# Kernel tuning notes

Hardware: AMD Instinct MI355X
Metric: run time of the kernel (lower is better)

Reference implementation:

```python
import jax, jax.numpy as jnp
import numpy as np
from jax import lax

B, C, H, W = 16, 128, 128, 128
K = 3
EPS = 1e-8


def setup_inputs() -> dict:
    key = jax.random.key(0)
    k1, k2, k3 = jax.random.split(key, 3)
    x = jax.random.normal(k1, (B, C, H, W), dtype=jnp.float32)
    style = jax.random.normal(k2, (B, C), dtype=jnp.float32)
    weight = jax.random.normal(k3, (C, C, K, K), dtype=jnp.float32)
    return {"x": x, "style": style, "weight": weight}


def reference(x, style, weight):
    b = x.shape[0]
    o, i, kh, kw = weight.shape
    h, w_sp = x.shape[2], x.shape[3]
    # style / ||style||_inf over channel dim (per-sample scalar)
    s = style / jnp.max(jnp.abs(style), axis=1, keepdims=True)          # (B, i)
    # weight * (1/sqrt(i*kh*kw)) / ||weight||_inf over (i,kh,kw) per out channel
    wmax = jnp.max(jnp.abs(weight), axis=(1, 2, 3), keepdims=True)      # (o,1,1,1)
    wn = weight * (1.0 / jnp.sqrt(jnp.float32(i * kh * kw)) / wmax)     # (o,i,kh,kw)
    # per-sample modulation over input channels
    wmod = wn[None] * s[:, None, :, None, None]                         # (B,o,i,kh,kw)
    # demodulation (coe reshaped to (i,1,1,1) in torch; valid since o==i)
    coe = lax.rsqrt(jnp.sum(jnp.square(wmod), axis=(2, 3, 4)) + EPS)    # (B,o)
    wmod = wmod * coe[:, :, None, None, None]
    # fused batched conv via grouped-conv trick (StyleGAN2-style)
    xr = x.reshape(1, b * i, h, w_sp)
    wr = wmod.reshape(b * o, i, kh, kw)
    out = lax.conv_general_dilated(
        xr, wr,
        window_strides=(1, 1),
        padding=[(1, 1), (1, 1)],
        feature_group_count=b,
        dimension_numbers=("NCHW", "OIHW", "NCHW"),
    )
    return out.reshape(b, o, h, w_sp)
```

## Files before the change

kernel.cpp:

```cpp
#include <hip/hip_runtime.h>
#include <hip/hip_bf16.h>


#define BATCH 16
#define CH    128
#define HW    128
#define WPITCH 1152

#define WS_WMAX 0
#define WS_SN   128
#define WS_AFAC 2176
#define WS_WT   4224
#define WFRAG_BYTE_OFF 606720
#define WFRAG_BYTES    4718592
#define WS_NEEDED      (WFRAG_BYTE_OFF + WFRAG_BYTES)

typedef short  s8v  __attribute__((ext_vector_type(8)));
typedef float  f4v  __attribute__((ext_vector_type(4)));
typedef float  f2v  __attribute__((ext_vector_type(2)));

__device__ inline unsigned short f2bf(float f) {
    union { float f; unsigned int u; } v; v.f = f;
    unsigned int r = v.u + 0x7FFFu + ((v.u >> 16) & 1u);
    return (unsigned short)(r >> 16);
}

__global__ __launch_bounds__(256) void kprep(const float* __restrict__ style,
                                             const float* __restrict__ weight,
                                             unsigned short* __restrict__ wfrag) {
    const int b  = blockIdx.x >> 3;
    const int mo = blockIdx.x & 7;
    const int t  = threadIdx.x;

    __shared__ float wrow[16 * 1153];
    __shared__ float snl[128];
    __shared__ float afl[16];
    __shared__ float red[4];

    float sv = (t < 128) ? style[b * CH + t] : 0.f;
    float m = fabsf(sv);
    #pragma unroll
    for (int off = 32; off > 0; off >>= 1)
        m = fmaxf(m, __shfl_down(m, off, 64));
    if ((t & 63) == 0) red[t >> 6] = m;

    for (int idx = t; idx < 16 * 1152; idx += 256) {
        int r = idx / 1152;
        int c = idx - r * 1152;
        wrow[r * 1153 + c] = weight[(size_t)(mo * 16 + r) * WPITCH + c];
    }
    __syncthreads();
    float smax = fmaxf(fmaxf(red[0], red[1]), fmaxf(red[2], red[3]));
    if (t < 128) snl[t] = sv / smax;
    __syncthreads();

    const int o16 = t >> 4;
    const int s   = t & 15;
    float mx = 0.f, ss = 0.f;
    for (int c = s; c < 1152; c += 16) {
        float v = wrow[o16 * 1153 + c];
        mx = fmaxf(mx, fabsf(v));
        float u = v * snl[c / 9];
        ss += u * u;
    }
    #pragma unroll
    for (int off = 8; off > 0; off >>= 1) {
        mx = fmaxf(mx, __shfl_down(mx, off, 16));
        ss += __shfl_down(ss, off, 16);
    }
    if (s == 0) {
        float scale = 1.0f / (sqrtf(1152.0f) * mx);
        afl[o16] = scale * rsqrtf(scale * scale * ss + 1e-8f);
    }
    __syncthreads();

    for (int fid = t; fid < 2304; fid += 256) {
        const int lane = fid & 63;
        int f2 = fid >> 6;
        const int ci = f2 & 3;
        const int kk = f2 >> 2;
        const int ro = lane & 15;
        const int i0 = ci * 32 + (lane >> 4) * 8;
        const float af = afl[ro];
        union { unsigned short u[8]; uint4 v; } pk;
        #pragma unroll
        for (int j = 0; j < 8; ++j) {
            int i = i0 + j;
            float v = wrow[ro * 1153 + i * 9 + kk] * af * snl[i];
            pk.u[j] = f2bf(v);
        }
        *(uint4*)(wfrag + ((size_t)(((b * 9 + kk) * 4 + ci) * 8 + mo) * 64 + lane) * 8) = pk.v;
    }
}

#define XBUF 16640

__device__ inline int xoff(int r, int c, int qs) { return (r * 130 + c) * 32 + qs * 8; }

__device__ inline const s8v* afrag_ptr(const unsigned short* wfrag, int b, int kk,
                                       int ci, int mo, int lane) {
    return (const s8v*)(wfrag + ((size_t)(((b * 9 + kk) * 4 + ci) * 8 + mo) * 64 + lane) * 8);
}

__global__ __launch_bounds__(512, 1) void k4_mfma(const float* __restrict__ x,
                                                  const unsigned short* __restrict__ wfrag,
                                                  float* __restrict__ out) {
    const int wg  = blockIdx.x;
    const int swz = (wg & 7) * 128 + (wg >> 3);
    const int b   = swz >> 6;
    const int h0  = (swz & 63) * 2;

    const int t    = threadIdx.x;
    const int lane = t & 63;
    const int wid  = t >> 6;
    const int oq    = wid & 3;
    const int rsel  = wid >> 2;
    const int ln15  = lane & 15;
    const int quad  = lane >> 4;

    __shared__ unsigned short xls[2 * XBUF];

    if (t < 64) {
        const int zb = (t >> 5) & 1;
        const int zr = (t >> 3) & 3;
        const int zc = ((t >> 2) & 1) ? 129 : 0;
        const int zq = t & 3;
        *(s8v*)&xls[zb * XBUF + xoff(zr, zc, zq)] = (s8v){0, 0, 0, 0, 0, 0, 0, 0};
    }

    f4v acc[2][8];
    #pragma unroll
    for (int mt = 0; mt < 2; ++mt)
        #pragma unroll
        for (int nt = 0; nt < 8; ++nt)
            acc[mt][nt] = (f4v){0.f, 0.f, 0.f, 0.f};

    const int  cp     = lane;
    const int  sr     = wid & 3;
    const int  hs     = wid >> 2;
    const int  it0    = hs * 2;
    const int  it1    = hs * 2 + 1;
    const int  srow   = h0 - 1 + sr;
    const bool svalid = (unsigned)srow < 128u;
    const int  srcl   = svalid ? srow : 0;

    #pragma unroll
    for (int k = 0; k < 2; ++k) {
        const int it = it0 + k;
        const float* xp = x + (((size_t)(b * CH + it * 8)) * HW + srcl) * HW + 2 * cp;
        union { unsigned short u[16]; s8v v[2]; } pk;
        #pragma unroll
        for (int j = 0; j < 8; ++j) {
            f2v d = *(const f2v*)(xp + (size_t)j * HW * HW);
            pk.u[j]     = f2bf(svalid ? d.x : 0.f);
            pk.u[8 + j] = f2bf(svalid ? d.y : 0.f);
        }
        *(s8v*)&xls[xoff(sr, 2 * cp + 1, it ^ (cp & 3))]       = pk.v[0];
        *(s8v*)&xls[xoff(sr, 2 * cp + 2, it ^ ((cp + 1) & 3))] = pk.v[1];
    }
    __syncthreads();

#define ISSUE(IT) do { \
    const float* xp_ = x + (((size_t)(b * CH + ibn + (IT) * 8)) * HW + srcl) * HW + 2 * cp; \
    _Pragma("unroll") \
    for (int j = 0; j < 8; ++j) pf[j] = *(const f2v*)(xp_ + (size_t)j * HW * HW); \
} while (0)

#define COMMIT(IT) do { \
    union { unsigned short u[16]; s8v v[2]; } pk_; \
    _Pragma("unroll") \
    for (int j = 0; j < 8; ++j) { \
        pk_.u[j]     = f2bf(svalid ? pf[j].x : 0.f); \
        pk_.u[8 + j] = f2bf(svalid ? pf[j].y : 0.f); } \
    *(s8v*)&bufn[xoff(sr, 2 * cp + 1, (IT) ^ (cp & 3))]       = pk_.v[0]; \
    *(s8v*)&bufn[xoff(sr, 2 * cp + 2, (IT) ^ ((cp + 1) & 3))] = pk_.v[1]; \
} while (0)

    s8v aN[2];
    #pragma unroll
    for (int mt = 0; mt < 2; ++mt)
        aN[mt] = *afrag_ptr(wfrag, b, 0, 0, oq * 2 + mt, lane);

    #pragma unroll 1
    for (int ci = 0; ci < 4; ++ci) {
        unsigned short* bufc = xls + (ci & 1) * XBUF;
        unsigned short* bufn = xls + ((ci & 1) ^ 1) * XBUF;
        const int ibn = (ci + 1) * 32;
        f2v pf[8];

        #pragma unroll
        for (int kk = 0; kk < 9; ++kk) {
            s8v aC[2];
            #pragma unroll
            for (int mt = 0; mt < 2; ++mt) aC[mt] = aN[mt];
            {
                const int pci = (kk < 8) ? ci : ci + 1;
                const int pkk = (kk < 8) ? kk + 1 : 0;
                if (pci < 4) {
                    #pragma unroll
                    for (int mt = 0; mt < 2; ++mt)
                        aN[mt] = *afrag_ptr(wfrag, b, pkk, pci, oq * 2 + mt, lane);
                }
            }
            if (ci < 3) {
                if      (kk == 0) { ISSUE(it0); }
                else if (kk == 4) { COMMIT(it0); ISSUE(it1); }
                else if (kk == 8) { COMMIT(it1); }
            }
            const int ky = kk / 3;
            const int kx = kk - ky * 3;
            const int r  = rsel + ky;
            s8v bf[8];
            #pragma unroll
            for (int nt = 0; nt < 8; ++nt) {
                const int c = nt * 16 + ln15 + kx;
                bf[nt] = *(const s8v*)&bufc[xoff(r, c, quad ^ ((c >> 1) & 3))];
            }
            #pragma unroll
            for (int mt = 0; mt < 2; ++mt)
                #pragma unroll
                for (int nt = 0; nt < 8; ++nt)
                    acc[mt][nt] = __builtin_amdgcn_mfma_f32_16x16x32_bf16(
                        aC[mt], bf[nt], acc[mt][nt], 0, 0, 0);
        }
        __syncthreads();
    }
#undef ISSUE
#undef COMMIT

    const int orow = h0 + rsel;
    #pragma unroll
    for (int mt = 0; mt < 2; ++mt) {
        int o = oq * 32 + mt * 16 + quad * 4;
        #pragma unroll
        for (int nt = 0; nt < 8; ++nt) {
            int xcol = nt * 16 + ln15;
            float* op = out + (((size_t)(b * CH + o)) * HW + orow) * HW + xcol;
            #pragma unroll
            for (int reg = 0; reg < 4; ++reg)
                op[(size_t)reg * HW * HW] = acc[mt][nt][reg];
        }
    }
}

__global__ __launch_bounds__(256) void k0_transpose(const float* __restrict__ w,
                                                    float* __restrict__ ws) {
    int idx = blockIdx.x * 256 + threadIdx.x;
    if (idx < CH * WPITCH) {
        int kt = idx >> 7;
        int o  = idx & 127;
        ws[WS_WT + idx] = w[(size_t)o * WPITCH + kt];
    }
}

__global__ __launch_bounds__(256) void k1_norms(const float* __restrict__ style,
                                                const float* __restrict__ weight,
                                                float* __restrict__ ws) {
    __shared__ float red[4];
    const int bid = blockIdx.x;
    const int t = threadIdx.x;
    if (bid < 128) {
        const int o = bid;
        float m = 0.f;
        for (int idx = t; idx < WPITCH; idx += 256)
            m = fmaxf(m, fabsf(weight[(size_t)o * WPITCH + idx]));
        #pragma unroll
        for (int off = 32; off > 0; off >>= 1)
            m = fmaxf(m, __shfl_down(m, off, 64));
        if ((t & 63) == 0) red[t >> 6] = m;
        __syncthreads();
        if (t == 0)
            ws[WS_WMAX + o] = fmaxf(fmaxf(red[0], red[1]), fmaxf(red[2], red[3]));
    } else {
        const int b = bid - 128;
        float v = (t < CH) ? style[b * CH + t] : 0.f;
        float m = fabsf(v);
        #pragma unroll
        for (int off = 32; off > 0; off >>= 1)
            m = fmaxf(m, __shfl_down(m, off, 64));
        if ((t & 63) == 0) red[t >> 6] = m;
        __syncthreads();
        float smax = fmaxf(fmaxf(red[0], red[1]), fmaxf(red[2], red[3]));
        if (t < CH) ws[WS_SN + b * CH + t] = v / smax;
    }
}

__global__ __launch_bounds__(256) void k2_coe(const float* __restrict__ weight,
                                              float* __restrict__ ws) {
    const int o = blockIdx.x;
    const int b = blockIdx.y;
    const int t = threadIdx.x;
    const float* sn = ws + WS_SN + b * CH;
    float s = 0.f;
    for (int idx = t; idx < WPITCH; idx += 256) {
        int i = idx / 9;
        float v = weight[(size_t)o * WPITCH + idx] * sn[i];
        s += v * v;
    }
    #pragma unroll
    for (int off = 32; off > 0; off >>= 1) s += __shfl_down(s, off, 64);
    __shared__ float red[4];
    if ((t & 63) == 0) red[t >> 6] = s;
    __syncthreads();
    if (t == 0) {
        float S = red[0] + red[1] + red[2] + red[3];
        float wm = ws[WS_WMAX + o];
        float scale = 1.0f / (sqrtf(1152.0f) * wm);
        float coe = rsqrtf(scale * scale * S + 1e-8f);
        ws[WS_AFAC + b * CH + o] = scale * coe;
    }
}

#define TI    8
#define XPITCH 132
__global__ __launch_bounds__(256) void k3_conv(const float* __restrict__ x,
                                               const float* __restrict__ ws,
                                               float* __restrict__ out) {
    const int h = blockIdx.x;
    const int b = blockIdx.y;
    const int t = threadIdx.x;
    const int og = t >> 4;
    const int pg = t & 15;

    __shared__ float x_lds[TI * 3 * XPITCH];
    __shared__ float w_lds[TI * 9 * 128];
    __shared__ float Af_l[128];
    __shared__ float sn_l[128];

    if (t < 128) {
        Af_l[t] = ws[WS_AFAC + b * CH + t];
        sn_l[t] = ws[WS_SN + b * CH + t];
    }
    float acc[8][8];
    #pragma unroll
    for (int j = 0; j < 8; ++j)
        #pragma unroll
        for (int p = 0; p < 8; ++p) acc[j][p] = 0.f;

    const float4* wt4 = (const float4*)(ws + WS_WT);
    float4* w_lds4 = (float4*)w_lds;
    const float4* Af4 = (const float4*)Af_l;

    #pragma unroll 1
    for (int ci = 0; ci < CH / TI; ++ci) {
        const int ib = ci * TI;
        __syncthreads();
        for (int idx = t; idx < TI * 3 * 130; idx += 256) {
            int ti  = idx / 390;
            int rem = idx - ti * 390;
            int r   = rem / 130;
            int c   = rem - r * 130;
            int row = h + r - 1;
            int col = c - 1;
            float v = 0.f;
            if ((unsigned)row < 128u && (unsigned)col < 128u)
                v = x[(((size_t)b * CH + ib + ti) * HW + row) * HW + col];
            x_lds[(ti * 3 + r) * XPITCH + c] = v;
        }
        for (int idx = t; idx < TI * 9 * 32; idx += 256) {
            int kt = idx >> 5;
            int o4 = idx & 31;
            int ti = kt / 9;
            float4 wv = wt4[(size_t)ib * 9 * 32 + idx];
            float4 af = Af4[o4];
            float  s  = sn_l[ib + ti];
            float4 rr;
            rr.x = wv.x * af.x * s; rr.y = wv.y * af.y * s;
            rr.z = wv.z * af.z * s; rr.w = wv.w * af.w * s;
            w_lds4[idx] = rr;
        }
        __syncthreads();
        #pragma unroll 1
        for (int ti = 0; ti < TI; ++ti) {
            float xv[3][12];
            #pragma unroll
            for (int ky = 0; ky < 3; ++ky)
                #pragma unroll
                for (int q = 0; q < 3; ++q) {
                    float4 v = *(const float4*)&x_lds[(ti * 3 + ky) * XPITCH + pg * 8 + q * 4];
                    xv[ky][q*4+0] = v.x; xv[ky][q*4+1] = v.y;
                    xv[ky][q*4+2] = v.z; xv[ky][q*4+3] = v.w;
                }
            #pragma unroll
            for (int kk = 0; kk < 9; ++kk) {
                const int ky = kk / 3;
                const int kx = kk % 3;
                float wv[8];
                #pragma unroll
                for (int q = 0; q < 2; ++q) {
                    float4 v = *(const float4*)&w_lds[(ti * 9 + kk) * 128 + og * 8 + q * 4];
                    wv[q*4+0] = v.x; wv[q*4+1] = v.y; wv[q*4+2] = v.z; wv[q*4+3] = v.w;
                }
                #pragma unroll
                for (int j = 0; j < 8; ++j)
                    #pragma unroll
                    for (int p = 0; p < 8; ++p)
                        acc[j][p] = fmaf(wv[j], xv[ky][p + kx], acc[j][p]);
            }
        }
    }
    const size_t obase = ((size_t)b * CH) * (HW * HW) + (size_t)h * HW;
    #pragma unroll
    for (int j = 0; j < 8; ++j) {
        int o = og * 8 + j;
        float4 v0 = {acc[j][0], acc[j][1], acc[j][2], acc[j][3]};
        float4 v1 = {acc[j][4], acc[j][5], acc[j][6], acc[j][7]};
        *(float4*)&out[obase + (size_t)o * (HW * HW) + pg * 8]     = v0;
        *(float4*)&out[obase + (size_t)o * (HW * HW) + pg * 8 + 4] = v1;
    }
}

extern "C" void kernel_launch(void* const* d_in, const int* in_sizes, int n_in,
                              void* d_out, int out_size, void* d_ws, size_t ws_size,
                              hipStream_t stream) {
    const float* x      = (const float*)d_in[0];
    const float* style  = (const float*)d_in[1];
    const float* weight = (const float*)d_in[2];
    float* out = (float*)d_out;
    float* ws  = (float*)d_ws;

    if (ws_size >= (size_t)WS_NEEDED) {
        unsigned short* wfrag = (unsigned short*)((char*)d_ws + WFRAG_BYTE_OFF);
        kprep<<<128, 256, 0, stream>>>(style, weight, wfrag);
        k4_mfma<<<1024, 512, 0, stream>>>(x, wfrag, out);
    } else {
        k0_transpose<<<(CH * WPITCH + 255) / 256, 256, 0, stream>>>(weight, ws);
        k1_norms<<<144, 256, 0, stream>>>(style, weight, ws);
        k2_coe<<<dim3(CH, BATCH), 256, 0, stream>>>(weight, ws);
        k3_conv<<<dim3(HW, BATCH), 256, 0, stream>>>(x, ws, out);
    }
}
```

Measured before the change: 298.3 us.

## Retile warps to 64x64 output blocks and double-buffer LDS B-fragment loads

Changes the per-wave tile from 32 output channels by 128 columns to 64 output channels by 64 columns, so each wave loads 4 A fragments and 4 B fragments per tap instead of 2 and 8. This lowers LDS read traffic per MFMA and balances global weight-fragment loads against LDS reads. It also prefetches the next tap's B fragments from LDS before the current tap's MFMAs, to hide LDS latency. The cost is more registers, from the extra A and B fragment buffers.

```diff
diff --git a/kernel.cpp b/kernel.cpp
--- a/kernel.cpp
+++ b/kernel.cpp
@@ -113,8 +113,9 @@
     const int t    = threadIdx.x;
     const int lane = t & 63;
     const int wid  = t >> 6;
-    const int oq    = wid & 3;
-    const int rsel  = wid >> 2;
+    const int ohalf   = wid & 1;
+    const int colhalf = (wid >> 1) & 1;
+    const int rsel    = wid >> 2;
     const int ln15  = lane & 15;
     const int quad  = lane >> 4;
 
@@ -128,11 +129,11 @@
         *(s8v*)&xls[zb * XBUF + xoff(zr, zc, zq)] = (s8v){0, 0, 0, 0, 0, 0, 0, 0};
     }
 
-    f4v acc[2][8];
-    #pragma unroll
-    for (int mt = 0; mt < 2; ++mt)
-        #pragma unroll
-        for (int nt = 0; nt < 8; ++nt)
+    f4v acc[4][4];
+    #pragma unroll
+    for (int mt = 0; mt < 4; ++mt)
+        #pragma unroll
+        for (int nt = 0; nt < 4; ++nt)
             acc[mt][nt] = (f4v){0.f, 0.f, 0.f, 0.f};
 
     const int  cp     = lane;
@@ -176,10 +177,19 @@
     *(s8v*)&bufn[xoff(sr, 2 * cp + 2, (IT) ^ ((cp + 1) & 3))] = pk_.v[1]; \
 } while (0)
 
-    s8v aN[2];
-    #pragma unroll
-    for (int mt = 0; mt < 2; ++mt)
-        aN[mt] = *afrag_ptr(wfrag, b, 0, 0, oq * 2 + mt, lane);
+#define LOADB(DST, KY, KX) do { \
+    const int r_ = rsel + (KY); \
+    _Pragma("unroll") \
+    for (int nt = 0; nt < 4; ++nt) { \
+        const int c_ = colhalf * 64 + nt * 16 + ln15 + (KX); \
+        (DST)[nt] = *(const s8v*)&bufc[xoff(r_, c_, quad ^ ((c_ >> 1) & 3))]; \
+    } \
+} while (0)
+
+    s8v aN[4];
+    #pragma unroll
+    for (int mt = 0; mt < 4; ++mt)
+        aN[mt] = *afrag_ptr(wfrag, b, 0, 0, ohalf * 4 + mt, lane);
 
     #pragma unroll 1
     for (int ci = 0; ci < 4; ++ci) {
@@ -188,18 +198,26 @@
         const int ibn = (ci + 1) * 32;
         f2v pf[8];
 
+        s8v bfC[4], bfN[4];
+        LOADB(bfC, 0, 0);
+
         #pragma unroll
         for (int kk = 0; kk < 9; ++kk) {
-            s8v aC[2];
-            #pragma unroll
-            for (int mt = 0; mt < 2; ++mt) aC[mt] = aN[mt];
+            if (kk < 8) {
+                const int nky = (kk + 1) / 3;
+                const int nkx = (kk + 1) - nky * 3;
+                LOADB(bfN, nky, nkx);
+            }
+            s8v aC[4];
+            #pragma unroll
+            for (int mt = 0; mt < 4; ++mt) aC[mt] = aN[mt];
             {
                 const int pci = (kk < 8) ? ci : ci + 1;
                 const int pkk = (kk < 8) ? kk + 1 : 0;
                 if (pci < 4) {
                     #pragma unroll
-                    for (int mt = 0; mt < 2; ++mt)
-                        aN[mt] = *afrag_ptr(wfrag, b, pkk, pci, oq * 2 + mt, lane);
+                    for (int mt = 0; mt < 4; ++mt)
+                        aN[mt] = *afrag_ptr(wfrag, b, pkk, pci, ohalf * 4 + mt, lane);
                 }
             }
             if (ci < 3) {
@@ -207,34 +225,28 @@
                 else if (kk == 4) { COMMIT(it0); ISSUE(it1); }
                 else if (kk == 8) { COMMIT(it1); }
             }
-            const int ky = kk / 3;
-            const int kx = kk - ky * 3;
-            const int r  = rsel + ky;
-            s8v bf[8];
-            #pragma unroll
-            for (int nt = 0; nt < 8; ++nt) {
-                const int c = nt * 16 + ln15 + kx;
-                bf[nt] = *(const s8v*)&bufc[xoff(r, c, quad ^ ((c >> 1) & 3))];
-            }
-            #pragma unroll
-            for (int mt = 0; mt < 2; ++mt)
+            #pragma unroll
+            for (int mt = 0; mt < 4; ++mt)
                 #pragma unroll
-                for (int nt = 0; nt < 8; ++nt)
+                for (int nt = 0; nt < 4; ++nt)
                     acc[mt][nt] = __builtin_amdgcn_mfma_f32_16x16x32_bf16(
-                        aC[mt], bf[nt], acc[mt][nt], 0, 0, 0);
+                        aC[mt], bfC[nt], acc[mt][nt], 0, 0, 0);
+            #pragma unroll
+            for (int nt = 0; nt < 4; ++nt) bfC[nt] = bfN[nt];
         }
         __syncthreads();
     }
 #undef ISSUE
 #undef COMMIT
+#undef LOADB
 
     const int orow = h0 + rsel;
     #pragma unroll
-    for (int mt = 0; mt < 2; ++mt) {
-        int o = oq * 32 + mt * 16 + quad * 4;
-        #pragma unroll
-        for (int nt = 0; nt < 8; ++nt) {
-            int xcol = nt * 16 + ln15;
+    for (int mt = 0; mt < 4; ++mt) {
+        int o = ohalf * 64 + mt * 16 + quad * 4;
+        #pragma unroll
+        for (int nt = 0; nt < 4; ++nt) {
+            int xcol = colhalf * 64 + nt * 16 + ln15;
             float* op = out + (((size_t)(b * CH + o)) * HW + orow) * HW + xcol;
             #pragma unroll
             for (int reg = 0; reg < 4; ++reg)
```

Result: no change. 298.4 us (+0.0%).

## Shrink MFMA conv tile to one output row per 256-thread block

Applied to the files above, without the earlier changes.

Each block now computes a single output row for all 128 output channels with 4 waves instead of two rows with 8 waves, using a 3-row LDS halo buffer. The launch becomes 2048 blocks of 256 threads with two blocks per CU, and the staging schedule loads three halo rows per channel chunk across the kernel taps. It also raises wave priority around the MFMA burst. The aim is better occupancy and latency hiding, at the cost of more redundant halo loads from global memory (3 rows per output row instead of 4 per 2).

```diff
diff --git a/kernel.cpp b/kernel.cpp
--- a/kernel.cpp
+++ b/kernel.cpp
@@ -93,7 +93,7 @@
     }
 }
 
-#define XBUF 16640
+#define XBUF 12480
 
 __device__ inline int xoff(int r, int c, int qs) { return (r * 130 + c) * 32 + qs * 8; }
 
@@ -102,29 +102,28 @@
     return (const s8v*)(wfrag + ((size_t)(((b * 9 + kk) * 4 + ci) * 8 + mo) * 64 + lane) * 8);
 }
 
-__global__ __launch_bounds__(512, 1) void k4_mfma(const float* __restrict__ x,
+__global__ __launch_bounds__(256, 2) void k4_mfma(const float* __restrict__ x,
                                                   const unsigned short* __restrict__ wfrag,
                                                   float* __restrict__ out) {
     const int wg  = blockIdx.x;
-    const int swz = (wg & 7) * 128 + (wg >> 3);
-    const int b   = swz >> 6;
-    const int h0  = (swz & 63) * 2;
+    const int swz = (wg & 7) * 256 + (wg >> 3);
+    const int b   = swz >> 7;
+    const int h   = swz & 127;
 
     const int t    = threadIdx.x;
     const int lane = t & 63;
-    const int wid  = t >> 6;
-    const int oq    = wid & 3;
-    const int rsel  = wid >> 2;
-    const int ln15  = lane & 15;
-    const int quad  = lane >> 4;
+    const int oq   = t >> 6;
+    const int ln15 = lane & 15;
+    const int quad = lane >> 4;
 
     __shared__ unsigned short xls[2 * XBUF];
 
-    if (t < 64) {
-        const int zb = (t >> 5) & 1;
-        const int zr = (t >> 3) & 3;
-        const int zc = ((t >> 2) & 1) ? 129 : 0;
-        const int zq = t & 3;
+    if (t < 48) {
+        int u = t;
+        const int zb = u / 24;  u -= zb * 24;
+        const int zr = u >> 3;
+        const int zc = ((u >> 2) & 1) ? 129 : 0;
+        const int zq = u & 3;
         *(s8v*)&xls[zb * XBUF + xoff(zr, zc, zq)] = (s8v){0, 0, 0, 0, 0, 0, 0, 0};
     }
 
@@ -135,45 +134,46 @@
         for (int nt = 0; nt < 8; ++nt)
             acc[mt][nt] = (f4v){0.f, 0.f, 0.f, 0.f};
 
-    const int  cp     = lane;
-    const int  sr     = wid & 3;
-    const int  hs     = wid >> 2;
-    const int  it0    = hs * 2;
-    const int  it1    = hs * 2 + 1;
-    const int  srow   = h0 - 1 + sr;
-    const bool svalid = (unsigned)srow < 128u;
-    const int  srcl   = svalid ? srow : 0;
-
-    #pragma unroll
-    for (int k = 0; k < 2; ++k) {
-        const int it = it0 + k;
-        const float* xp = x + (((size_t)(b * CH + it * 8)) * HW + srcl) * HW + 2 * cp;
-        union { unsigned short u[16]; s8v v[2]; } pk;
-        #pragma unroll
-        for (int j = 0; j < 8; ++j) {
-            f2v d = *(const f2v*)(xp + (size_t)j * HW * HW);
-            pk.u[j]     = f2bf(svalid ? d.x : 0.f);
-            pk.u[8 + j] = f2bf(svalid ? d.y : 0.f);
-        }
-        *(s8v*)&xls[xoff(sr, 2 * cp + 1, it ^ (cp & 3))]       = pk.v[0];
-        *(s8v*)&xls[xoff(sr, 2 * cp + 2, it ^ ((cp + 1) & 3))] = pk.v[1];
+    const int cp = (t >> 2) & 63;
+    const int g  = t & 3;
+    const bool sv0 = (h - 1) >= 0;
+    const bool sv2 = (h + 1) < 128;
+    const int  sc0 = sv0 ? h - 1 : 0;
+    const int  sc2 = sv2 ? h + 1 : 0;
+
+    {
+        const bool svs[3] = {sv0, true, sv2};
+        const int  scs[3] = {sc0, h, sc2};
+        #pragma unroll
+        for (int s = 0; s < 3; ++s) {
+            const float* xp = x + (((size_t)(b * CH + g * 8)) * HW + scs[s]) * HW + 2 * cp;
+            union { unsigned short u[16]; s8v v[2]; } pk;
+            #pragma unroll
+            for (int j = 0; j < 8; ++j) {
+                f2v d = *(const f2v*)(xp + (size_t)j * HW * HW);
+                pk.u[j]     = f2bf(svs[s] ? d.x : 0.f);
+                pk.u[8 + j] = f2bf(svs[s] ? d.y : 0.f);
+            }
+            *(s8v*)&xls[xoff(s, 2 * cp + 1, g ^ (cp & 3))]       = pk.v[0];
+            *(s8v*)&xls[xoff(s, 2 * cp + 2, g ^ ((cp + 1) & 3))] = pk.v[1];
+        }
     }
     __syncthreads();
 
-#define ISSUE(IT) do { \
-    const float* xp_ = x + (((size_t)(b * CH + ibn + (IT) * 8)) * HW + srcl) * HW + 2 * cp; \
+#define ISSUE(S, SV, SC) do { \
+    const float* xp_ = x + (((size_t)(b * CH + ibn + g * 8)) * HW + (SC)) * HW + 2 * cp; \
     _Pragma("unroll") \
     for (int j = 0; j < 8; ++j) pf[j] = *(const f2v*)(xp_ + (size_t)j * HW * HW); \
 } while (0)
 
-#define COMMIT(IT) do { \
+#define COMMIT(S, SV) do { \
     union { unsigned short u[16]; s8v v[2]; } pk_; \
     _Pragma("unroll") \
     for (int j = 0; j < 8; ++j) { \
-        pk_.u[j]     = f2bf(svalid ? pf[j].x : 0.f); \
-        pk_.u[8 + j] = f2bf(svalid ? pf[j].y : 0.f); } \
-    *(s8v*)&bufn[xoff(sr, 2 * cp + 1, (IT) ^ (cp & 3))]       = pk_.v[0]; \
-    *(s8v*)&bufn[xoff(sr, 2 * cp + 2, (IT) ^ ((cp + 1) & 3))] = pk_.v[1]; \
+        pk_.u[j]     = f2bf((SV) ? pf[j].x : 0.f); \
+        pk_.u[8 + j] = f2bf((SV) ? pf[j].y : 0.f); } \
+    *(s8v*)&bufn[xoff((S), 2 * cp + 1, g ^ (cp & 3))]       = pk_.v[0]; \
+    *(s8v*)&bufn[xoff((S), 2 * cp + 2, g ^ ((cp + 1) & 3))] = pk_.v[1]; \
 } while (0)
 
     s8v aN[2];
@@ -203,39 +203,40 @@
                 }
             }
             if (ci < 3) {
-                if      (kk == 0) { ISSUE(it0); }
-                else if (kk == 4) { COMMIT(it0); ISSUE(it1); }
-                else if (kk == 8) { COMMIT(it1); }
+                if      (kk == 0) { ISSUE(0, sv0, sc0); }
+                else if (kk == 3) { COMMIT(0, sv0); ISSUE(1, true, h); }
+                else if (kk == 6) { COMMIT(1, true); ISSUE(2, sv2, sc2); }
+                else if (kk == 8) { COMMIT(2, sv2); }
             }
             const int ky = kk / 3;
             const int kx = kk - ky * 3;
-            const int r  = rsel + ky;
             s8v bf[8];
             #pragma unroll
             for (int nt = 0; nt < 8; ++nt) {
                 const int c = nt * 16 + ln15 + kx;
-                bf[nt] = *(const s8v*)&bufc[xoff(r, c, quad ^ ((c >> 1) & 3))];
+                bf[nt] = *(const s8v*)&bufc[xoff(ky, c, quad ^ ((c >> 1) & 3))];
             }
+            __builtin_amdgcn_s_setprio(1);
             #pragma unroll
             for (int mt = 0; mt < 2; ++mt)
                 #pragma unroll
                 for (int nt = 0; nt < 8; ++nt)
                     acc[mt][nt] = __builtin_amdgcn_mfma_f32_16x16x32_bf16(
                         aC[mt], bf[nt], acc[mt][nt], 0, 0, 0);
+            __builtin_amdgcn_s_setprio(0);
         }
         __syncthreads();
     }
 #undef ISSUE
 #undef COMMIT
 
-    const int orow = h0 + rsel;
     #pragma unroll
     for (int mt = 0; mt < 2; ++mt) {
         int o = oq * 32 + mt * 16 + quad * 4;
         #pragma unroll
         for (int nt = 0; nt < 8; ++nt) {
             int xcol = nt * 16 + ln15;
-            float* op = out + (((size_t)(b * CH + o)) * HW + orow) * HW + xcol;
+            float* op = out + (((size_t)(b * CH + o)) * HW + h) * HW + xcol;
             #pragma unroll
             for (int reg = 0; reg < 4; ++reg)
                 op[(size_t)reg * HW * HW] = acc[mt][nt][reg];
@@ -422,7 +423,7 @@
     if (ws_size >= (size_t)WS_NEEDED) {
         unsigned short* wfrag = (unsigned short*)((char*)d_ws + WFRAG_BYTE_OFF);
         kprep<<<128, 256, 0, stream>>>(style, weight, wfrag);
-        k4_mfma<<<1024, 512, 0, stream>>>(x, wfrag, out);
+        k4_mfma<<<2048, 256, 0, stream>>>(x, wfrag, out);
     } else {
         k0_transpose<<<(CH * WPITCH + 255) / 256, 256, 0, stream>>>(weight, ws);
         k1_norms<<<144, 256, 0, stream>>>(style, weight, ws);
```

After: 331.0 us. 1.11x slower.
